# Performance work log

Measured on AMD Instinct MI355X. Metric: run time of the kernel, lower is better.

Reference implementation:

```python
import jax, jax.numpy as jnp
import numpy as np

D_MODEL = 512
D_FF = 2048
NUM_EXPERTS = 8
TOP_K = 2


def setup_inputs() -> dict:
    key = jax.random.key(0)
    ks = jax.random.split(key, 6)
    scale = 0.02
    x = jax.random.normal(ks[0], (4, 8192, D_MODEL), dtype=jnp.float32)
    gate_w = jax.random.normal(ks[1], (D_MODEL, NUM_EXPERTS), dtype=jnp.float32) * scale
    w1 = jax.random.normal(ks[2], (NUM_EXPERTS, D_MODEL, D_FF), dtype=jnp.float32) * scale
    b1 = jnp.zeros((NUM_EXPERTS, D_FF), dtype=jnp.float32)
    w2 = jax.random.normal(ks[3], (NUM_EXPERTS, D_FF, D_MODEL), dtype=jnp.float32) * scale
    b2 = jnp.zeros((NUM_EXPERTS, D_MODEL), dtype=jnp.float32)
    return {"x": x, "gate_w": gate_w, "w1": w1, "b1": b1, "w2": w2, "b2": b2}


def reference(x, gate_w, w1, b1, w2, b2):
    B, S, D = x.shape
    xt = x.reshape(-1, D)                                  # [T, D]
    logits = xt @ gate_w                                   # [T, E]
    probs = jax.nn.softmax(logits, axis=-1)
    top_p, top_i = jax.lax.top_k(probs, TOP_K)             # [T, K]
    top_p = top_p / jnp.sum(top_p, axis=-1, keepdims=True)
    # per-token combine weight for each expert: [T, E]
    w_te = jnp.sum(jax.nn.one_hot(top_i, NUM_EXPERTS, dtype=xt.dtype) * top_p[..., None], axis=1)
    out = jnp.zeros_like(xt)
    for e in range(NUM_EXPERTS):  # small fixed loop over experts
        h = jax.nn.gelu(xt @ w1[e] + b1[e], approximate=False)  # [T, d_ff]
        y = h @ w2[e] + b2[e]                                   # [T, D]
        out = out + w_te[:, e:e + 1] * y
    return out.reshape(B, S, D)
```

## Files before the change

kernel.cpp:

```cpp
#include <hip/hip_runtime.h>
#include <math.h>

#define T_TOK 32768
#define DM 512
#define DFF 2048
#define NE 8
#define MAXTILES 528

typedef __attribute__((ext_vector_type(8))) short short8;
typedef __attribute__((ext_vector_type(4))) float f32x4;

__device__ __forceinline__ unsigned int f2bf1(float f) {
  union { float f; unsigned int u; } x; x.f = f;
  return (x.u + 0x7fffu + ((x.u >> 16) & 1u)) >> 16;
}

#define GLOAD(src, dst) \
  __builtin_amdgcn_global_load_lds((const __attribute__((address_space(1))) unsigned int*)(src), \
                                   (__attribute__((address_space(3))) unsigned int*)(dst), 16, 0, 0)
#define WAITVM(N) asm volatile("s_waitcnt vmcnt(" #N ")" ::: "memory")
#define BARRIER() asm volatile("s_barrier" ::: "memory")

template <int PERM>
__global__ void tcvt_kernel(const float* __restrict__ src, unsigned short* __restrict__ dst,
                            int R, int C) {
  __shared__ float tile[32][33];
  int e = blockIdx.z;
  const float* s = src + (size_t)e * R * C;
  unsigned short* d = dst + (size_t)e * R * C;
  int c0 = blockIdx.x * 32, r0 = blockIdx.y * 32;
  int tx = threadIdx.x, ty = threadIdx.y;
#pragma unroll
  for (int i = 0; i < 4; ++i)
    tile[ty + i * 8][tx] = s[(size_t)(r0 + ty + i * 8) * C + c0 + tx];
  __syncthreads();
#pragma unroll
  for (int i = 0; i < 4; ++i) {
    int rr = r0 + tx;
    if (PERM) rr = (rr & ~31) | ((rr & 15) << 1) | ((rr >> 4) & 1);
    d[(size_t)(c0 + ty + i * 8) * R + rr] = (unsigned short)f2bf1(tile[tx][ty + i * 8]);
  }
}

__global__ __launch_bounds__(1024) void gate_kernel(
    const float* __restrict__ x, const float* __restrict__ gw,
    int* __restrict__ cnt, int* __restrict__ tok, float* __restrict__ wgt,
    unsigned int* __restrict__ xb) {
  __shared__ int lcnt[NE];
  __shared__ int lbase[NE];
  __shared__ int wslot[16][2];
  __shared__ int winfo[16][2];
  __shared__ float wval[16][2];
  int tid = threadIdx.x;
  int wid = tid >> 6, lane = tid & 63;
  int t = blockIdx.x * 16 + wid;
  if (tid < NE) lcnt[tid] = 0;
  __syncthreads();

  float acc[NE];
#pragma unroll
  for (int e = 0; e < NE; ++e) acc[e] = 0.f;
  const float* xr = x + (size_t)t * DM;
  unsigned int* xbr = xb + (size_t)t * (DM / 2);
#pragma unroll
  for (int j = 0; j < 4; ++j) {
    int d0 = j * 128 + lane * 2;
    float2 xv = *(const float2*)(xr + d0);
    const float* g0 = gw + d0 * NE;
#pragma unroll
    for (int e = 0; e < NE; ++e) acc[e] += xv.x * g0[e] + xv.y * g0[NE + e];
    xbr[j * 64 + lane] = f2bf1(xv.x) | (f2bf1(xv.y) << 16);
  }
#pragma unroll
  for (int off = 32; off >= 1; off >>= 1) {
#pragma unroll
    for (int e = 0; e < NE; ++e) acc[e] += __shfl_xor(acc[e], off);
  }
  if (lane == 0) {
    int e0 = 0; float l0 = acc[0];
#pragma unroll
    for (int e = 1; e < NE; ++e) if (acc[e] > l0) { l0 = acc[e]; e0 = e; }
    int e1 = (e0 == 0) ? 1 : 0; float l1 = acc[e1];
#pragma unroll
    for (int e = 0; e < NE; ++e) if (e != e0 && acc[e] > l1) { l1 = acc[e]; e1 = e; }
    float w0 = 1.f / (1.f + expf(l1 - l0));
    winfo[wid][0] = e0; winfo[wid][1] = e1;
    wval[wid][0] = w0;  wval[wid][1] = 1.f - w0;
    wslot[wid][0] = atomicAdd(&lcnt[e0], 1);
    wslot[wid][1] = atomicAdd(&lcnt[e1], 1);
  }
  __syncthreads();
  if (tid < NE) lbase[tid] = atomicAdd(&cnt[tid * 64], lcnt[tid]);
  __syncthreads();
  if (lane == 0) {
    int e0 = winfo[wid][0], e1 = winfo[wid][1];
    int p0 = lbase[e0] + wslot[wid][0];
    int p1 = lbase[e1] + wslot[wid][1];
    tok[e0 * T_TOK + p0] = t; wgt[e0 * T_TOK + p0] = wval[wid][0];
    tok[e1 * T_TOK + p1] = t; wgt[e1 * T_TOK + p1] = wval[wid][1];
  }
}

__global__ void plan_kernel(const int* __restrict__ cnt, int* __restrict__ tile_base) {
  if (threadIdx.x == 0 && blockIdx.x == 0) {
    int tb = 0;
    for (int e = 0; e < NE; ++e) { tile_base[e] = tb; tb += (cnt[e * 64] + 127) >> 7; }
    tile_base[NE] = tb;
  }
}

__global__ __launch_bounds__(256) void gemm1_kernel(
    const unsigned int* __restrict__ xb, const unsigned short* __restrict__ w1t,
    const float* __restrict__ b1, const int* __restrict__ cnt,
    const int* __restrict__ tok, const int* __restrict__ tile_base,
    unsigned short* __restrict__ H, int tile_lo) {
  int nwg = (int)gridDim.x;
  int bid0 = (int)blockIdx.x;
  int bid = (bid0 & 7) * (nwg >> 3) + (bid0 >> 3);
  int nt = bid & 15;
  int gt = tile_lo + (bid >> 4);
  if (gt >= tile_base[NE]) return;
  int e = 0;
#pragma unroll
  for (int k = 0; k < NE - 1; ++k) e += (gt >= tile_base[k + 1]) ? 1 : 0;
  int tloc = gt - tile_base[e];
  int ce = cnt[e * 64];
  int m0 = tloc * 128;
  int n0 = nt * 128;

  __shared__ char Lds[4 * 16384];

  int tid = (int)threadIdx.x;
  int lane = tid & 63;
  int wid = tid >> 6;
  int wm = wid & 1, wn = wid >> 1;
  int fl = lane & 15, q = lane >> 4;
  int sxy = ((q ^ ((fl >> 1) & 3)) << 4);

  const int* tokg = tok + e * T_TOK;
  int r0 = tid >> 2, r1 = 64 + (tid >> 2);
  int sl = tid & 3;
  int ss0 = sl ^ ((r0 >> 1) & 3);
  int ss1 = sl ^ ((r1 >> 1) & 3);
  int t0 = tokg[min(m0 + r0, ce - 1)];
  int t1 = tokg[min(m0 + r1, ce - 1)];
  const char* asrc0 = (const char*)xb + (size_t)t0 * 1024 + ss0 * 16;
  const char* asrc1 = (const char*)xb + (size_t)t1 * 1024 + ss1 * 16;
  const char* bsrc0 = (const char*)w1t + ((size_t)e * DFF + n0 + r0) * 1024 + ss0 * 16;
  const char* bsrc1 = (const char*)w1t + ((size_t)e * DFF + n0 + r1) * 1024 + ss1 * 16;

  int aoff[4], boff[4];
#pragma unroll
  for (int i = 0; i < 4; ++i) {
    aoff[i] = (wm * 64 + i * 16 + fl) * 64 + sxy;
    boff[i] = 8192 + (wn * 64 + i * 16 + fl) * 64 + sxy;
  }

  f32x4 acc[4][4];
#pragma unroll
  for (int a = 0; a < 4; ++a)
#pragma unroll
    for (int b = 0; b < 4; ++b) acc[a][b] = (f32x4){0.f, 0.f, 0.f, 0.f};

#define STAGE1(bi, ti) do { \
    char* base_ = Lds + (bi) * 16384; size_t ko_ = (size_t)(ti) * 64; \
    GLOAD(asrc0 + ko_, base_ + tid * 16);        \
    GLOAD(asrc1 + ko_, base_ + 4096 + tid * 16); \
    GLOAD(bsrc0 + ko_, base_ + 8192 + tid * 16); \
    GLOAD(bsrc1 + ko_, base_ + 12288 + tid * 16); } while (0)

#define COMP1(bi) do { \
    const char* base_ = Lds + (bi) * 16384; \
    short8 a[4], b[4]; \
    _Pragma("unroll") for (int i = 0; i < 4; ++i) { \
      a[i] = *(const short8*)(base_ + aoff[i]); \
      b[i] = *(const short8*)(base_ + boff[i]); } \
    __builtin_amdgcn_s_setprio(1); \
    _Pragma("unroll") for (int mf = 0; mf < 4; ++mf) \
    _Pragma("unroll") for (int nf = 0; nf < 4; ++nf) \
      acc[mf][nf] = __builtin_amdgcn_mfma_f32_16x16x32_bf16(a[mf], b[nf], acc[mf][nf], 0, 0, 0); \
    __builtin_amdgcn_s_setprio(0); \
  } while (0)

#define STEP1(t, sb, cb) do { \
    WAITVM(8); BARRIER(); STAGE1(sb, (t) + 3); COMP1(cb); } while (0)

  STAGE1(0, 0); STAGE1(1, 1); STAGE1(2, 2);
  for (int tt = 0; tt < 12; tt += 4) {
    STEP1(tt + 0, 3, 0);
    STEP1(tt + 1, 0, 1);
    STEP1(tt + 2, 1, 2);
    STEP1(tt + 3, 2, 3);
  }
  WAITVM(8); BARRIER(); STAGE1(3, 15); COMP1(0);
  WAITVM(8); BARRIER(); COMP1(1);
  WAITVM(4); BARRIER(); COMP1(2);
  WAITVM(0); BARRIER(); COMP1(3);
#undef STEP1
#undef STAGE1
#undef COMP1

  size_t hrow0 = (size_t)(gt - tile_lo) * 128;
  float bv[4];
#pragma unroll
  for (int nf = 0; nf < 4; ++nf) bv[nf] = b1[e * DFF + n0 + wn * 64 + nf * 16 + fl];
#pragma unroll
  for (int mf = 0; mf < 4; ++mf)
#pragma unroll
    for (int j = 0; j < 4; ++j) {
      int row = wm * 64 + mf * 16 + q * 4 + j;
      float g[4];
#pragma unroll
      for (int nf = 0; nf < 4; ++nf) {
        float v = acc[mf][nf][j] + bv[nf];
        float u2 = v * (1.5957691216f + 0.0713548162f * v * v);
        g[nf] = v / (1.f + __expf(-u2));
      }
      unsigned int* Hp = (unsigned int*)(H + (hrow0 + row) * DFF + n0 + wn * 64);
      Hp[fl]      = f2bf1(g[0]) | (f2bf1(g[1]) << 16);
      Hp[16 + fl] = f2bf1(g[2]) | (f2bf1(g[3]) << 16);
    }
}

__global__ __launch_bounds__(256) void gemm2_kernel(
    const unsigned short* __restrict__ H, const unsigned short* __restrict__ w2t,
    const float* __restrict__ b2, const int* __restrict__ cnt,
    const int* __restrict__ tok, const float* __restrict__ wgt,
    const int* __restrict__ tile_base, float* __restrict__ out, int tile_lo) {
  int nwg = (int)gridDim.x;
  int bid0 = (int)blockIdx.x;
  int bid = (bid0 & 7) * (nwg >> 3) + (bid0 >> 3);
  int nt = bid & 3;
  int gt = tile_lo + (bid >> 2);
  if (gt >= tile_base[NE]) return;
  int e = 0;
#pragma unroll
  for (int k = 0; k < NE - 1; ++k) e += (gt >= tile_base[k + 1]) ? 1 : 0;
  int tloc = gt - tile_base[e];
  int ce = cnt[e * 64];
  int m0 = tloc * 128;
  int n0 = nt * 128;

  __shared__ char Lds[4 * 16384];

  int tid = (int)threadIdx.x;
  int lane = tid & 63;
  int wid = tid >> 6;
  int wm = wid & 1, wn = wid >> 1;
  int fl = lane & 15, q = lane >> 4;
  int sxy = ((q ^ ((fl >> 1) & 3)) << 4);

  int r0 = tid >> 2, r1 = 64 + (tid >> 2);
  int sl = tid & 3;
  int ss0 = sl ^ ((r0 >> 1) & 3);
  int ss1 = sl ^ ((r1 >> 1) & 3);
  size_t hrow0 = (size_t)(gt - tile_lo) * 128;
  const char* asrc0 = (const char*)H + (hrow0 + r0) * 4096 + ss0 * 16;
  const char* asrc1 = (const char*)H + (hrow0 + r1) * 4096 + ss1 * 16;
  const char* bsrc0 = (const char*)w2t + ((size_t)e * DM + n0 + r0) * 4096 + ss0 * 16;
  const char* bsrc1 = (const char*)w2t + ((size_t)e * DM + n0 + r1) * 4096 + ss1 * 16;

  int aoff[4], boff[4];
#pragma unroll
  for (int i = 0; i < 4; ++i) {
    aoff[i] = (wm * 64 + i * 16 + fl) * 64 + sxy;
    boff[i] = 8192 + (wn * 64 + i * 16 + fl) * 64 + sxy;
  }

  f32x4 acc[4][4];
#pragma unroll
  for (int a = 0; a < 4; ++a)
#pragma unroll
    for (int b = 0; b < 4; ++b) acc[a][b] = (f32x4){0.f, 0.f, 0.f, 0.f};

#define STAGE2(bi, ti) do { \
    char* base_ = Lds + (bi) * 16384; size_t ko_ = (size_t)(ti) * 64; \
    GLOAD(asrc0 + ko_, base_ + tid * 16);        \
    GLOAD(asrc1 + ko_, base_ + 4096 + tid * 16); \
    GLOAD(bsrc0 + ko_, base_ + 8192 + tid * 16); \
    GLOAD(bsrc1 + ko_, base_ + 12288 + tid * 16); } while (0)

#define COMP2(bi) do { \
    const char* base_ = Lds + (bi) * 16384; \
    short8 a[4], b[4]; \
    _Pragma("unroll") for (int i = 0; i < 4; ++i) { \
      a[i] = *(const short8*)(base_ + aoff[i]); \
      b[i] = *(const short8*)(base_ + boff[i]); } \
    __builtin_amdgcn_s_setprio(1); \
    _Pragma("unroll") for (int mf = 0; mf < 4; ++mf) \
    _Pragma("unroll") for (int nf = 0; nf < 4; ++nf) \
      acc[mf][nf] = __builtin_amdgcn_mfma_f32_16x16x32_bf16(a[mf], b[nf], acc[mf][nf], 0, 0, 0); \
    __builtin_amdgcn_s_setprio(0); \
  } while (0)

#define STEP2(t, sb, cb) do { \
    WAITVM(8); BARRIER(); STAGE2(sb, (t) + 3); COMP2(cb); } while (0)

  STAGE2(0, 0); STAGE2(1, 1); STAGE2(2, 2);
  for (int tt = 0; tt < 60; tt += 4) {
    STEP2(tt + 0, 3, 0);
    STEP2(tt + 1, 0, 1);
    STEP2(tt + 2, 1, 2);
    STEP2(tt + 3, 2, 3);
  }
  WAITVM(8); BARRIER(); STAGE2(3, 63); COMP2(0);
  WAITVM(8); BARRIER(); COMP2(1);
  WAITVM(4); BARRIER(); COMP2(2);
  WAITVM(0); BARRIER(); COMP2(3);
#undef STEP2
#undef STAGE2
#undef COMP2

  const int* tokg = tok + e * T_TOK;
  const float* wgtg = wgt + e * T_TOK;
  float bias2[4];
#pragma unroll
  for (int nf = 0; nf < 4; ++nf) bias2[nf] = b2[e * DM + n0 + wn * 64 + nf * 16 + fl];
#pragma unroll
  for (int mf = 0; mf < 4; ++mf)
#pragma unroll
    for (int j = 0; j < 4; ++j) {
      int row = wm * 64 + mf * 16 + q * 4 + j;
      int slot = m0 + row;
      if (slot < ce) {
        int tk = tokg[slot];
        float w = wgtg[slot];
        float* orow = out + (size_t)tk * DM + n0 + wn * 64;
#pragma unroll
        for (int nf = 0; nf < 4; ++nf)
          atomicAdd(orow + nf * 16 + fl, w * (acc[mf][nf][j] + bias2[nf]));
      }
    }
}

extern "C" void kernel_launch(void* const* d_in, const int* in_sizes, int n_in,
                              void* d_out, int out_size, void* d_ws, size_t ws_size,
                              hipStream_t stream) {
  (void)in_sizes; (void)n_in; (void)out_size;
  const float* x  = (const float*)d_in[0];
  const float* gw = (const float*)d_in[1];
  const float* w1 = (const float*)d_in[2];
  const float* b1 = (const float*)d_in[3];
  const float* w2 = (const float*)d_in[4];
  const float* b2 = (const float*)d_in[5];
  float* out = (float*)d_out;

  char* ws = (char*)d_ws;
  size_t off = 0;
  auto alloc = [&](size_t sz) { char* p = ws + off; off += (sz + 255) & ~(size_t)255; return p; };
  int*   cnt = (int*)alloc(NE * 64 * 4);
  int*   tok = (int*)alloc((size_t)NE * T_TOK * 4);
  float* wgt = (float*)alloc((size_t)NE * T_TOK * 4);
  int*   tile_base = (int*)alloc((NE + 1) * 4);
  unsigned int* xb = (unsigned int*)alloc((size_t)T_TOK * (DM / 2) * 4);
  unsigned short* w1t = (unsigned short*)alloc((size_t)NE * DFF * DM * 2);
  unsigned short* w2t = (unsigned short*)alloc((size_t)NE * DM * DFF * 2);

  size_t avail = (ws_size > off) ? (ws_size - off) : 0;
  int TPC = MAXTILES, NC = 1;
  while (NC < 32 && (size_t)TPC * 128 * DFF * 2 > avail) {
    NC *= 2;
    TPC = (((MAXTILES + NC - 1) / NC) + 1) & ~1;
  }
  unsigned short* H = (unsigned short*)alloc((size_t)TPC * 128 * DFF * 2);

  hipMemsetAsync(cnt, 0, NE * 64 * 4, stream);
  hipMemsetAsync(out, 0, (size_t)T_TOK * DM * 4, stream);

  tcvt_kernel<0><<<dim3(DFF / 32, DM / 32, NE), dim3(32, 8), 0, stream>>>(w1, w1t, DM, DFF);
  tcvt_kernel<1><<<dim3(DM / 32, DFF / 32, NE), dim3(32, 8), 0, stream>>>(w2, w2t, DFF, DM);
  gate_kernel<<<T_TOK / 16, 1024, 0, stream>>>(x, gw, cnt, tok, wgt, xb);
  plan_kernel<<<1, 64, 0, stream>>>(cnt, tile_base);

  for (int c = 0; c * TPC < MAXTILES; ++c) {
    int lo = c * TPC;
    gemm1_kernel<<<TPC * 16, 256, 0, stream>>>(xb, w1t, b1, cnt, tok, tile_base, H, lo);
    gemm2_kernel<<<TPC * 4, 256, 0, stream>>>(H, w2t, b2, cnt, tok, wgt, tile_base, out, lo);
  }
}
```

Before: 582.4 us.

## Enlarge GEMM M-tile to 256 rows with triple-buffered LDS pipeline

Both grouped GEMMs now use 256x128 output tiles, with each wave computing 128x64 (8x4 MFMA fragments), instead of 128x128. This raises arithmetic intensity per weight tile and halves the number of tiles. The LDS pipeline drops from 4 stages to 3 to fit the larger per-stage buffers, launch bounds request 2 workgroups per CU, and the setprio hints are removed. The trade-offs are more padding waste in partially filled expert tiles, higher register pressure from 32 accumulators, fewer workgroups to fill the machine, and a shallower prefetch depth.

```diff
diff --git a/kernel.cpp b/kernel.cpp
--- a/kernel.cpp
+++ b/kernel.cpp
@@ -5,7 +5,7 @@
 #define DM 512
 #define DFF 2048
 #define NE 8
-#define MAXTILES 528
+#define MAXT 264
 
 typedef __attribute__((ext_vector_type(8))) short short8;
 typedef __attribute__((ext_vector_type(4))) float f32x4;
@@ -104,12 +104,12 @@
 __global__ void plan_kernel(const int* __restrict__ cnt, int* __restrict__ tile_base) {
   if (threadIdx.x == 0 && blockIdx.x == 0) {
     int tb = 0;
-    for (int e = 0; e < NE; ++e) { tile_base[e] = tb; tb += (cnt[e * 64] + 127) >> 7; }
+    for (int e = 0; e < NE; ++e) { tile_base[e] = tb; tb += (cnt[e * 64] + 255) >> 8; }
     tile_base[NE] = tb;
   }
 }
 
-__global__ __launch_bounds__(256) void gemm1_kernel(
+__global__ __launch_bounds__(256, 2) void gemm1_kernel(
     const unsigned int* __restrict__ xb, const unsigned short* __restrict__ w1t,
     const float* __restrict__ b1, const int* __restrict__ cnt,
     const int* __restrict__ tok, const int* __restrict__ tile_base,
@@ -125,10 +125,10 @@
   for (int k = 0; k < NE - 1; ++k) e += (gt >= tile_base[k + 1]) ? 1 : 0;
   int tloc = gt - tile_base[e];
   int ce = cnt[e * 64];
-  int m0 = tloc * 128;
+  int m0 = tloc * 256;
   int n0 = nt * 128;
 
-  __shared__ char Lds[4 * 16384];
+  __shared__ char Lds[3 * 24576];
 
   int tid = (int)threadIdx.x;
   int lane = tid & 63;
@@ -138,77 +138,71 @@
   int sxy = ((q ^ ((fl >> 1) & 3)) << 4);
 
   const int* tokg = tok + e * T_TOK;
-  int r0 = tid >> 2, r1 = 64 + (tid >> 2);
-  int sl = tid & 3;
-  int ss0 = sl ^ ((r0 >> 1) & 3);
-  int ss1 = sl ^ ((r1 >> 1) & 3);
-  int t0 = tokg[min(m0 + r0, ce - 1)];
-  int t1 = tokg[min(m0 + r1, ce - 1)];
-  const char* asrc0 = (const char*)xb + (size_t)t0 * 1024 + ss0 * 16;
-  const char* asrc1 = (const char*)xb + (size_t)t1 * 1024 + ss1 * 16;
-  const char* bsrc0 = (const char*)w1t + ((size_t)e * DFF + n0 + r0) * 1024 + ss0 * 16;
-  const char* bsrc1 = (const char*)w1t + ((size_t)e * DFF + n0 + r1) * 1024 + ss1 * 16;
-
-  int aoff[4], boff[4];
-#pragma unroll
-  for (int i = 0; i < 4; ++i) {
-    aoff[i] = (wm * 64 + i * 16 + fl) * 64 + sxy;
-    boff[i] = 8192 + (wn * 64 + i * 16 + fl) * 64 + sxy;
-  }
-
-  f32x4 acc[4][4];
-#pragma unroll
-  for (int a = 0; a < 4; ++a)
+  int r = tid >> 2, sl = tid & 3;
+  int ss = sl ^ ((r >> 1) & 3);
+  const char* asrc[4];
+#pragma unroll
+  for (int g = 0; g < 4; ++g) {
+    int tk = tokg[min(m0 + g * 64 + r, ce - 1)];
+    asrc[g] = (const char*)xb + (size_t)tk * 1024 + ss * 16;
+  }
+  const char* bsrc[2];
+#pragma unroll
+  for (int g = 0; g < 2; ++g)
+    bsrc[g] = (const char*)w1t + ((size_t)e * DFF + n0 + g * 64 + r) * 1024 + ss * 16;
+
+  int aoff[8], boff[4];
+#pragma unroll
+  for (int i = 0; i < 8; ++i) aoff[i] = (wm * 128 + i * 16 + fl) * 64 + sxy;
+#pragma unroll
+  for (int j = 0; j < 4; ++j) boff[j] = 16384 + (wn * 64 + j * 16 + fl) * 64 + sxy;
+
+  f32x4 acc[8][4];
+#pragma unroll
+  for (int a = 0; a < 8; ++a)
 #pragma unroll
     for (int b = 0; b < 4; ++b) acc[a][b] = (f32x4){0.f, 0.f, 0.f, 0.f};
 
 #define STAGE1(bi, ti) do { \
-    char* base_ = Lds + (bi) * 16384; size_t ko_ = (size_t)(ti) * 64; \
-    GLOAD(asrc0 + ko_, base_ + tid * 16);        \
-    GLOAD(asrc1 + ko_, base_ + 4096 + tid * 16); \
-    GLOAD(bsrc0 + ko_, base_ + 8192 + tid * 16); \
-    GLOAD(bsrc1 + ko_, base_ + 12288 + tid * 16); } while (0)
+    char* base_ = Lds + (bi) * 24576; size_t ko_ = (size_t)(ti) * 64; \
+    GLOAD(asrc[0] + ko_, base_ + tid * 16);          \
+    GLOAD(asrc[1] + ko_, base_ + 4096 + tid * 16);   \
+    GLOAD(asrc[2] + ko_, base_ + 8192 + tid * 16);   \
+    GLOAD(asrc[3] + ko_, base_ + 12288 + tid * 16);  \
+    GLOAD(bsrc[0] + ko_, base_ + 16384 + tid * 16);  \
+    GLOAD(bsrc[1] + ko_, base_ + 20480 + tid * 16); } while (0)
 
 #define COMP1(bi) do { \
-    const char* base_ = Lds + (bi) * 16384; \
-    short8 a[4], b[4]; \
-    _Pragma("unroll") for (int i = 0; i < 4; ++i) { \
-      a[i] = *(const short8*)(base_ + aoff[i]); \
-      b[i] = *(const short8*)(base_ + boff[i]); } \
-    __builtin_amdgcn_s_setprio(1); \
-    _Pragma("unroll") for (int mf = 0; mf < 4; ++mf) \
+    const char* base_ = Lds + (bi) * 24576; \
+    short8 a[8], b[4]; \
+    _Pragma("unroll") for (int i = 0; i < 8; ++i) a[i] = *(const short8*)(base_ + aoff[i]); \
+    _Pragma("unroll") for (int j = 0; j < 4; ++j) b[j] = *(const short8*)(base_ + boff[j]); \
+    _Pragma("unroll") for (int mf = 0; mf < 8; ++mf) \
     _Pragma("unroll") for (int nf = 0; nf < 4; ++nf) \
       acc[mf][nf] = __builtin_amdgcn_mfma_f32_16x16x32_bf16(a[mf], b[nf], acc[mf][nf], 0, 0, 0); \
-    __builtin_amdgcn_s_setprio(0); \
   } while (0)
 
-#define STEP1(t, sb, cb) do { \
-    WAITVM(8); BARRIER(); STAGE1(sb, (t) + 3); COMP1(cb); } while (0)
-
-  STAGE1(0, 0); STAGE1(1, 1); STAGE1(2, 2);
-  for (int tt = 0; tt < 12; tt += 4) {
-    STEP1(tt + 0, 3, 0);
-    STEP1(tt + 1, 0, 1);
-    STEP1(tt + 2, 1, 2);
-    STEP1(tt + 3, 2, 3);
-  }
-  WAITVM(8); BARRIER(); STAGE1(3, 15); COMP1(0);
-  WAITVM(8); BARRIER(); COMP1(1);
-  WAITVM(4); BARRIER(); COMP1(2);
-  WAITVM(0); BARRIER(); COMP1(3);
-#undef STEP1
+  STAGE1(0, 0); STAGE1(1, 1);
+  for (int t = 0; t < 14; ++t) {
+    WAITVM(6);
+    BARRIER();
+    STAGE1((t + 2) % 3, t + 2);
+    COMP1(t % 3);
+  }
+  WAITVM(6); BARRIER(); COMP1(14 % 3);
+  WAITVM(0); BARRIER(); COMP1(15 % 3);
 #undef STAGE1
 #undef COMP1
 
-  size_t hrow0 = (size_t)(gt - tile_lo) * 128;
+  size_t hrow0 = (size_t)(gt - tile_lo) * 256;
   float bv[4];
 #pragma unroll
   for (int nf = 0; nf < 4; ++nf) bv[nf] = b1[e * DFF + n0 + wn * 64 + nf * 16 + fl];
 #pragma unroll
-  for (int mf = 0; mf < 4; ++mf)
+  for (int mf = 0; mf < 8; ++mf)
 #pragma unroll
     for (int j = 0; j < 4; ++j) {
-      int row = wm * 64 + mf * 16 + q * 4 + j;
+      int row = wm * 128 + mf * 16 + q * 4 + j;
       float g[4];
 #pragma unroll
       for (int nf = 0; nf < 4; ++nf) {
@@ -222,7 +216,7 @@
     }
 }
 
-__global__ __launch_bounds__(256) void gemm2_kernel(
+__global__ __launch_bounds__(256, 2) void gemm2_kernel(
     const unsigned short* __restrict__ H, const unsigned short* __restrict__ w2t,
     const float* __restrict__ b2, const int* __restrict__ cnt,
     const int* __restrict__ tok, const float* __restrict__ wgt,
@@ -238,10 +232,10 @@
   for (int k = 0; k < NE - 1; ++k) e += (gt >= tile_base[k + 1]) ? 1 : 0;
   int tloc = gt - tile_base[e];
   int ce = cnt[e * 64];
-  int m0 = tloc * 128;
+  int m0 = tloc * 256;
   int n0 = nt * 128;
 
-  __shared__ char Lds[4 * 16384];
+  __shared__ char Lds[3 * 24576];
 
   int tid = (int)threadIdx.x;
   int lane = tid & 63;
@@ -250,64 +244,58 @@
   int fl = lane & 15, q = lane >> 4;
   int sxy = ((q ^ ((fl >> 1) & 3)) << 4);
 
-  int r0 = tid >> 2, r1 = 64 + (tid >> 2);
-  int sl = tid & 3;
-  int ss0 = sl ^ ((r0 >> 1) & 3);
-  int ss1 = sl ^ ((r1 >> 1) & 3);
-  size_t hrow0 = (size_t)(gt - tile_lo) * 128;
-  const char* asrc0 = (const char*)H + (hrow0 + r0) * 4096 + ss0 * 16;
-  const char* asrc1 = (const char*)H + (hrow0 + r1) * 4096 + ss1 * 16;
-  const char* bsrc0 = (const char*)w2t + ((size_t)e * DM + n0 + r0) * 4096 + ss0 * 16;
-  const char* bsrc1 = (const char*)w2t + ((size_t)e * DM + n0 + r1) * 4096 + ss1 * 16;
-
-  int aoff[4], boff[4];
-#pragma unroll
-  for (int i = 0; i < 4; ++i) {
-    aoff[i] = (wm * 64 + i * 16 + fl) * 64 + sxy;
-    boff[i] = 8192 + (wn * 64 + i * 16 + fl) * 64 + sxy;
-  }
-
-  f32x4 acc[4][4];
-#pragma unroll
-  for (int a = 0; a < 4; ++a)
+  int r = tid >> 2, sl = tid & 3;
+  int ss = sl ^ ((r >> 1) & 3);
+  size_t hrow0 = (size_t)(gt - tile_lo) * 256;
+  const char* asrc[4];
+#pragma unroll
+  for (int g = 0; g < 4; ++g)
+    asrc[g] = (const char*)H + (hrow0 + g * 64 + r) * 4096 + ss * 16;
+  const char* bsrc[2];
+#pragma unroll
+  for (int g = 0; g < 2; ++g)
+    bsrc[g] = (const char*)w2t + ((size_t)e * DM + n0 + g * 64 + r) * 4096 + ss * 16;
+
+  int aoff[8], boff[4];
+#pragma unroll
+  for (int i = 0; i < 8; ++i) aoff[i] = (wm * 128 + i * 16 + fl) * 64 + sxy;
+#pragma unroll
+  for (int j = 0; j < 4; ++j) boff[j] = 16384 + (wn * 64 + j * 16 + fl) * 64 + sxy;
+
+  f32x4 acc[8][4];
+#pragma unroll
+  for (int a = 0; a < 8; ++a)
 #pragma unroll
     for (int b = 0; b < 4; ++b) acc[a][b] = (f32x4){0.f, 0.f, 0.f, 0.f};
 
 #define STAGE2(bi, ti) do { \
-    char* base_ = Lds + (bi) * 16384; size_t ko_ = (size_t)(ti) * 64; \
-    GLOAD(asrc0 + ko_, base_ + tid * 16);        \
-    GLOAD(asrc1 + ko_, base_ + 4096 + tid * 16); \
-    GLOAD(bsrc0 + ko_, base_ + 8192 + tid * 16); \
-    GLOAD(bsrc1 + ko_, base_ + 12288 + tid * 16); } while (0)
+    char* base_ = Lds + (bi) * 24576; size_t ko_ = (size_t)(ti) * 64; \
+    GLOAD(asrc[0] + ko_, base_ + tid * 16);          \
+    GLOAD(asrc[1] + ko_, base_ + 4096 + tid * 16);   \
+    GLOAD(asrc[2] + ko_, base_ + 8192 + tid * 16);   \
+    GLOAD(asrc[3] + ko_, base_ + 12288 + tid * 16);  \
+    GLOAD(bsrc[0] + ko_, base_ + 16384 + tid * 16);  \
+    GLOAD(bsrc[1] + ko_, base_ + 20480 + tid * 16); } while (0)
 
 #define COMP2(bi) do { \
-    const char* base_ = Lds + (bi) * 16384; \
-    short8 a[4], b[4]; \
-    _Pragma("unroll") for (int i = 0; i < 4; ++i) { \
-      a[i] = *(const short8*)(base_ + aoff[i]); \
-      b[i] = *(const short8*)(base_ + boff[i]); } \
-    __builtin_amdgcn_s_setprio(1); \
-    _Pragma("unroll") for (int mf = 0; mf < 4; ++mf) \
+    const char* base_ = Lds + (bi) * 24576; \
+    short8 a[8], b[4]; \
+    _Pragma("unroll") for (int i = 0; i < 8; ++i) a[i] = *(const short8*)(base_ + aoff[i]); \
+    _Pragma("unroll") for (int j = 0; j < 4; ++j) b[j] = *(const short8*)(base_ + boff[j]); \
+    _Pragma("unroll") for (int mf = 0; mf < 8; ++mf) \
     _Pragma("unroll") for (int nf = 0; nf < 4; ++nf) \
       acc[mf][nf] = __builtin_amdgcn_mfma_f32_16x16x32_bf16(a[mf], b[nf], acc[mf][nf], 0, 0, 0); \
-    __builtin_amdgcn_s_setprio(0); \
   } while (0)
 
-#define STEP2(t, sb, cb) do { \
-    WAITVM(8); BARRIER(); STAGE2(sb, (t) + 3); COMP2(cb); } while (0)
-
-  STAGE2(0, 0); STAGE2(1, 1); STAGE2(2, 2);
-  for (int tt = 0; tt < 60; tt += 4) {
-    STEP2(tt + 0, 3, 0);
-    STEP2(tt + 1, 0, 1);
-    STEP2(tt + 2, 1, 2);
-    STEP2(tt + 3, 2, 3);
-  }
-  WAITVM(8); BARRIER(); STAGE2(3, 63); COMP2(0);
-  WAITVM(8); BARRIER(); COMP2(1);
-  WAITVM(4); BARRIER(); COMP2(2);
-  WAITVM(0); BARRIER(); COMP2(3);
-#undef STEP2
+  STAGE2(0, 0); STAGE2(1, 1);
+  for (int t = 0; t < 62; ++t) {
+    WAITVM(6);
+    BARRIER();
+    STAGE2((t + 2) % 3, t + 2);
+    COMP2(t % 3);
+  }
+  WAITVM(6); BARRIER(); COMP2(62 % 3);
+  WAITVM(0); BARRIER(); COMP2(63 % 3);
 #undef STAGE2
 #undef COMP2
 
@@ -317,10 +305,10 @@
 #pragma unroll
   for (int nf = 0; nf < 4; ++nf) bias2[nf] = b2[e * DM + n0 + wn * 64 + nf * 16 + fl];
 #pragma unroll
-  for (int mf = 0; mf < 4; ++mf)
+  for (int mf = 0; mf < 8; ++mf)
 #pragma unroll
     for (int j = 0; j < 4; ++j) {
-      int row = wm * 64 + mf * 16 + q * 4 + j;
+      int row = wm * 128 + mf * 16 + q * 4 + j;
       int slot = m0 + row;
       if (slot < ce) {
         int tk = tokg[slot];
@@ -357,12 +345,12 @@
   unsigned short* w2t = (unsigned short*)alloc((size_t)NE * DM * DFF * 2);
 
   size_t avail = (ws_size > off) ? (ws_size - off) : 0;
-  int TPC = MAXTILES, NC = 1;
-  while (NC < 32 && (size_t)TPC * 128 * DFF * 2 > avail) {
+  int TPC = MAXT, NC = 1;
+  while (NC < 32 && (size_t)TPC * 256 * DFF * 2 > avail) {
     NC *= 2;
-    TPC = (((MAXTILES + NC - 1) / NC) + 1) & ~1;
-  }
-  unsigned short* H = (unsigned short*)alloc((size_t)TPC * 128 * DFF * 2);
+    TPC = (((MAXT + NC - 1) / NC) + 1) & ~1;
+  }
+  unsigned short* H = (unsigned short*)alloc((size_t)TPC * 256 * DFF * 2);
 
   hipMemsetAsync(cnt, 0, NE * 64 * 4, stream);
   hipMemsetAsync(out, 0, (size_t)T_TOK * DM * 4, stream);
@@ -372,7 +360,7 @@
   gate_kernel<<<T_TOK / 16, 1024, 0, stream>>>(x, gw, cnt, tok, wgt, xb);
   plan_kernel<<<1, 64, 0, stream>>>(cnt, tile_base);
 
-  for (int c = 0; c * TPC < MAXTILES; ++c) {
+  for (int c = 0; c * TPC < MAXT; ++c) {
     int lo = c * TPC;
     gemm1_kernel<<<TPC * 16, 256, 0, stream>>>(xb, w1t, b1, cnt, tok, tile_base, H, lo);
     gemm2_kernel<<<TPC * 4, 256, 0, stream>>>(H, w2t, b2, cnt, tok, wgt, tile_base, out, lo);
```

Measured after the change: 614.9 us. +5.6%, slower.
